# Optimization experiments

Measured on AMD Instinct MI355X. Metric: run time of the kernel, lower is better.

## Reference

```python
import jax, jax.numpy as jnp
import numpy as np

B, T, D = 512, 720, 774
P, H, E = 128, 128, 64


def setup_inputs() -> dict:
    key = jax.random.key(0)
    ks = jax.random.split(key, 24)
    x = jax.random.normal(ks[0], (B, T, D), jnp.float32)
    # emulate days with no news (all-zero rows) so has_news/recency are non-trivial
    news_mask = jax.random.bernoulli(ks[1], 0.35, (B, T, 1)).astype(jnp.float32)
    x = x * news_mask

    def w(k, shape, s=0.05):
        return jax.random.normal(k, shape, jnp.float32) * s

    return {
        "x": x,
        "w_proj": w(ks[2], (D + 2, P)), "b_proj": jnp.zeros((P,), jnp.float32),
        "ln_g": jnp.ones((P,), jnp.float32), "ln_b": jnp.zeros((P,), jnp.float32),
        # LSTM params stored as (in, 4H) / (H, 4H); torch gate order i,f,g,o
        "wih0": w(ks[3], (P, 4 * H)), "whh0": w(ks[4], (H, 4 * H)),
        "bih0": jnp.zeros((4 * H,), jnp.float32), "bhh0": jnp.zeros((4 * H,), jnp.float32).at[H:2 * H].set(1.0),
        "wih1": w(ks[5], (H, 4 * H)), "whh1": w(ks[6], (H, 4 * H)),
        "bih1": jnp.zeros((4 * H,), jnp.float32), "bhh1": jnp.zeros((4 * H,), jnp.float32).at[H:2 * H].set(1.0),
        "w_e1": w(ks[7], (H, H)), "b_e1": jnp.zeros((H,), jnp.float32),
        "w_e2": w(ks[8], (H, E)), "b_e2": jnp.zeros((E,), jnp.float32),
        "w_r": w(ks[9], (H, H // 2)), "b_r": jnp.zeros((H // 2,), jnp.float32),
        "w_o": w(ks[10], (H // 2, 1)), "b_o": jnp.zeros((1,), jnp.float32),
        "w_s": w(ks[11], (H, 1)),
    }


def _lstm_layer(inp, Wih, Whh, bih, bhh):
    # inp: (B, T, Din) -> (B, T, H). Precompute input projection once (GEMM),
    # scan only the recurrent part.
    b = inp.shape[0]
    h_dim = Whh.shape[0]
    pre = jnp.swapaxes(inp, 0, 1) @ Wih + bih + bhh  # (T, B, 4H)

    def step(carry, pt):
        h, c = carry
        g = pt + h @ Whh
        i, f, gg, o = jnp.split(g, 4, axis=-1)
        c = jax.nn.sigmoid(f) * c + jax.nn.sigmoid(i) * jnp.tanh(gg)
        h = jax.nn.sigmoid(o) * jnp.tanh(c)
        return (h, c), h

    init = (jnp.zeros((b, h_dim), inp.dtype), jnp.zeros((b, h_dim), inp.dtype))
    _, hs = jax.lax.scan(step, init, pre)
    return jnp.swapaxes(hs, 0, 1)  # (B, T, H)


def reference(x, w_proj, b_proj, ln_g, ln_b,
              wih0, whh0, bih0, bhh0, wih1, whh1, bih1, bhh1,
              w_e1, b_e1, w_e2, b_e2, w_r, b_r, w_o, b_o, w_s):
    t = x.shape[1]
    has = (jnp.sum(jnp.abs(x), axis=-1, keepdims=True) > 1e-6).astype(x.dtype)  # (B,T,1)
    # recency: days since last news / T -- the 720-step python loop is exactly
    # a reset-cumsum == (t - last_news_index)/T with last index from a cummax
    t_idx = jnp.arange(t, dtype=x.dtype)[None, :, None]
    last = jax.lax.cummax(jnp.where(has > 0.5, t_idx, jnp.float32(-1.0)), axis=1)
    rec = jnp.clip((t_idx - last) / t, 0.0, 1.0)

    xa = jnp.concatenate([x, has, rec], axis=-1)  # (B,T,D+2)
    h = jax.nn.gelu(xa @ w_proj + b_proj, approximate=False)  # dropout=eval no-op
    mu = jnp.mean(h, axis=-1, keepdims=True)
    var = jnp.var(h, axis=-1, keepdims=True)
    h = (h - mu) / jnp.sqrt(var + 1e-5) * ln_g + ln_b

    h = _lstm_layer(h, wih0, whh0, bih0, bhh0)
    h = _lstm_layer(h, wih1, whh1, bih1, bhh1)
    last_h = h[:, -1, :]  # (B,H)

    emb = jnp.tanh(jax.nn.gelu(last_h @ w_e1 + b_e1, approximate=False) @ w_e2 + b_e2)
    hr = jax.nn.gelu(last_h @ w_r + b_r, approximate=False)
    pred = (hr @ w_o + b_o + last_h @ w_s)[:, 0]
    return pred, emb
```

## Files before the change

### kernel.cpp

```cpp
#include <hip/hip_runtime.h>
#include <math.h>

#define BB 512
#define TT 720
#define DD 774
#define PP 128
#define HH 128
#define GG 512
#define DP2 776
#define TAB 721

__device__ __forceinline__ float gelu_f(float v){
    return 0.5f*v*(1.0f + erff(v*0.70710678118654752f));
}
__device__ __forceinline__ float sig_f(float v){
    return 1.0f/(1.0f + __expf(-v));
}

__global__ void k_zero(float* __restrict__ p, int n){
    int i = blockIdx.x*256 + threadIdx.x;
    if (i < n) p[i] = 0.f;
}

__global__ __launch_bounds__(256) void k_has(const float* __restrict__ x, float* __restrict__ has){
    int wid  = blockIdx.x*4 + (threadIdx.x >> 6);
    int lane = threadIdx.x & 63;
    const float2* row = reinterpret_cast<const float2*>(x + (size_t)wid*DD);
    float s = 0.f;
    #pragma unroll
    for (int i=0;i<6;i++){ float2 v = row[lane + i*64]; s += fabsf(v.x)+fabsf(v.y); }
    if (lane < 3){ float2 v = row[384 + lane]; s += fabsf(v.x)+fabsf(v.y); }
    #pragma unroll
    for (int off=32; off; off>>=1) s += __shfl_down(s, off, 64);
    if (lane == 0) has[wid] = (s > 1e-6f) ? 1.0f : 0.0f;
}

__global__ void k_rec(const float* __restrict__ has, int* __restrict__ recIdx,
                      int* __restrict__ cnt_bc, int Tc, int NC){
    int b = blockIdx.x*64 + threadIdx.x;
    if (b >= BB) return;
    const float* hp = has + (size_t)b*TT;
    int* rp = recIdx + (size_t)b*TT;
    int last = -1, cl = 0, c = 0;
    for (int t=0;t<TT;t++){
        if (t == (c+1)*Tc){ cnt_bc[b*NC + c] = cl; cl = 0; c++; }
        if (hp[t] > 0.5f){ last = t; cl++; }
        rp[t] = t - last;
    }
    cnt_bc[b*NC + c] = cl;
}

__global__ __launch_bounds__(512) void k_scan(const int* __restrict__ cnt_bc, int* __restrict__ base_bc,
                                              int* __restrict__ cntTotal, int NC){
    int c = blockIdx.x;
    int b = threadIdx.x;
    int v = cnt_bc[b*NC + c];
    int lane = b & 63, w = b >> 6;
    int xv = v;
    #pragma unroll
    for (int off=1; off<64; off<<=1){
        int y = __shfl_up(xv, off, 64);
        if (lane >= off) xv += y;
    }
    __shared__ int wsums[8];
    if (lane == 63) wsums[w] = xv;
    __syncthreads();
    if (b == 0){
        int run = 0;
        #pragma unroll
        for (int i=0;i<8;i++){ int tv = wsums[i]; wsums[i] = run; run += tv; }
        cntTotal[c] = run;
    }
    __syncthreads();
    base_bc[b*NC + c] = wsums[w] + xv - v;
}

__global__ void k_pos(const float* __restrict__ has, const int* __restrict__ base_bc,
                      int* __restrict__ posIdx, int* __restrict__ list, int Tc, int NC){
    int b = blockIdx.x*64 + threadIdx.x;
    if (b >= BB) return;
    const float* hp = has + (size_t)b*TT;
    int c = 0;
    int pos = base_bc[b*NC + 0];
    for (int t=0;t<TT;t++){
        if (t == (c+1)*Tc){ c++; pos = base_bc[b*NC + c]; }
        int r = b*TT + t;
        if (hp[t] > 0.5f){
            posIdx[r] = pos;
            list[(size_t)c*((size_t)BB*Tc) + pos] = r;
            pos++;
        } else {
            posIdx[r] = -1;
        }
    }
}

__global__ __launch_bounds__(128) void k_tab1(const float* __restrict__ wp, const float* __restrict__ bp,
        const float* __restrict__ lng, const float* __restrict__ lnb, float* __restrict__ tab1){
    int k = blockIdx.x, j = threadIdx.x;
    float rec = (float)k * (1.0f/720.0f);
    float v = gelu_f(rec * wp[775*PP + j] + bp[j]);
    int lane = j & 63, w = j >> 6;
    __shared__ float red[2];
    float s = v;
    #pragma unroll
    for (int off=32; off; off>>=1) s += __shfl_xor(s, off, 64);
    if (lane == 0) red[w] = s;
    __syncthreads();
    float mu = (red[0] + red[1]) * (1.0f/128.0f);
    __syncthreads();
    float d = v - mu, s2 = d*d;
    #pragma unroll
    for (int off=32; off; off>>=1) s2 += __shfl_xor(s2, off, 64);
    if (lane == 0) red[w] = s2;
    __syncthreads();
    float var = (red[0] + red[1]) * (1.0f/128.0f);
    tab1[k*PP + j] = d * rsqrtf(var + 1e-5f) * lng[j] + lnb[j];
}

__global__ __launch_bounds__(512) void k_tab2(const float* __restrict__ tab1, const float* __restrict__ wih,
        const float* __restrict__ bih, const float* __restrict__ bhh, float* __restrict__ tab2){
    int k = blockIdx.x, j = threadIdx.x;
    __shared__ float hrow[PP];
    if (j < PP) hrow[j] = tab1[k*PP + j];
    __syncthreads();
    float acc = bih[j] + bhh[j];
    #pragma unroll
    for (int kk=0; kk<PP; kk++) acc += hrow[kk]*wih[kk*GG + j];
    tab2[(size_t)k*GG + j] = acc;
}

__global__ __launch_bounds__(256) void k_proj(const float* __restrict__ x,
        const float* __restrict__ wp, const float* __restrict__ bp,
        const float* __restrict__ lng, const float* __restrict__ lnb,
        const int* __restrict__ listc, const int* __restrict__ cntPtr,
        float* __restrict__ h0c){
    int nc = cntPtr[0];
    int base = blockIdx.x*16;
    if (base >= nc) return;
    int nrows = min(16, nc - base);
    __shared__ float xs[16][DP2];
    __shared__ float hls[16][PP];
    __shared__ float mvs[16][2];
    const int tid = threadIdx.x;
    for (int rr=0; rr<16; rr++){
        if (rr < nrows){
            int row = listc[base + rr];
            const float* xr = x + (size_t)row*DD;
            for (int d = tid; d < DD; d += 256) xs[rr][d] = xr[d];
            if (tid == 0){ xs[rr][774] = 1.0f; xs[rr][775] = 0.0f; }
        }
    }
    __syncthreads();
    int col = tid & 127, rg = tid >> 7;
    float acc[8];
    #pragma unroll
    for (int r=0;r<8;r++) acc[r] = bp[col];
    const float* wcol = wp + col;
    for (int d=0; d<DP2; d+=4){
        float w0 = wcol[(d+0)*PP], w1 = wcol[(d+1)*PP], w2 = wcol[(d+2)*PP], w3 = wcol[(d+3)*PP];
        #pragma unroll
        for (int r=0;r<8;r++){
            float4 xv = *reinterpret_cast<const float4*>(&xs[rg*8 + r][d]);
            acc[r] = fmaf(xv.x, w0, acc[r]);
            acc[r] = fmaf(xv.y, w1, acc[r]);
            acc[r] = fmaf(xv.z, w2, acc[r]);
            acc[r] = fmaf(xv.w, w3, acc[r]);
        }
    }
    #pragma unroll
    for (int r=0;r<8;r++){ acc[r] = gelu_f(acc[r]); hls[rg*8 + r][col] = acc[r]; }
    __syncthreads();
    int w = tid >> 6, lane = tid & 63;
    for (int rr = w*4; rr < w*4 + 4; rr++){
        float s = hls[rr][lane] + hls[rr][lane + 64];
        #pragma unroll
        for (int off=32; off; off>>=1) s += __shfl_xor(s, off, 64);
        float mu = s * (1.0f/128.0f);
        float d0 = hls[rr][lane]-mu, d1 = hls[rr][lane+64]-mu;
        float s2 = d0*d0 + d1*d1;
        #pragma unroll
        for (int off=32; off; off>>=1) s2 += __shfl_xor(s2, off, 64);
        if (lane == 0){ mvs[rr][0] = mu; mvs[rr][1] = rsqrtf(s2*(1.0f/128.0f) + 1e-5f); }
    }
    __syncthreads();
    float g = lng[col], bb = lnb[col];
    #pragma unroll
    for (int r=0;r<8;r++){
        int rr = rg*8 + r;
        if (base + rr < nc){
            float o = (acc[r] - mvs[rr][0]) * mvs[rr][1] * g + bb;
            h0c[(size_t)(base+rr)*PP + col] = o;
        }
    }
}

__global__ __launch_bounds__(512) void k_pre(const float* __restrict__ inM,
        const float* __restrict__ wih, const float* __restrict__ bih, const float* __restrict__ bhh,
        const int* __restrict__ cntPtr, int fixedCount, float* __restrict__ outPre){
    int nc = cntPtr ? cntPtr[0] : fixedCount;
    int base = blockIdx.x*32;
    if (base >= nc) return;
    __shared__ float hs[32][PP];
    int tid = threadIdx.x;
    for (int i = tid; i < 32*PP; i += 512){
        int rr = i >> 7;
        if (base + rr < nc) hs[rr][i & 127] = inM[(size_t)(base+rr)*PP + (i & 127)];
    }
    __syncthreads();
    float bias = bih[tid] + bhh[tid];
    float acc[32];
    #pragma unroll
    for (int r=0;r<32;r++) acc[r] = bias;
    const float* wc = wih + tid;
    for (int k=0;k<PP;k+=4){
        float w0 = wc[(k+0)*GG], w1 = wc[(k+1)*GG], w2 = wc[(k+2)*GG], w3 = wc[(k+3)*GG];
        #pragma unroll
        for (int r=0;r<32;r++){
            float4 hv = *reinterpret_cast<const float4*>(&hs[r][k]);
            acc[r] = fmaf(hv.x, w0, acc[r]);
            acc[r] = fmaf(hv.y, w1, acc[r]);
            acc[r] = fmaf(hv.z, w2, acc[r]);
            acc[r] = fmaf(hv.w, w3, acc[r]);
        }
    }
    #pragma unroll
    for (int r=0;r<32;r++)
        if (base + r < nc) outPre[(size_t)(base+r)*GG + tid] = acc[r];
}

__global__ __launch_bounds__(512, 2) void k_lstm(
    const float* __restrict__ whh, const float* __restrict__ pre,
    const float* __restrict__ pretab, const int* __restrict__ posIdx,
    const int* __restrict__ recIdx, float* __restrict__ hState, float* __restrict__ cState,
    float* __restrict__ hsOut, int t0, int Tc, int layer)
{
    int b = blockIdx.x;
    int j = threadIdx.x;
    float w[128];
    #pragma unroll
    for (int k=0;k<128;k++) w[k] = whh[k*GG + j];
    __shared__ float hbuf[HH];
    __shared__ float hprev[HH];
    __shared__ float gbuf[GG];
    if (j < HH) hbuf[j] = hState[b*HH + j];
    float c_ = (j < HH) ? cState[b*HH + j] : 0.f;
    __syncthreads();
    for (int t = t0; t < t0 + Tc; t++){
        if (hsOut && t > t0 && j >= 128 && j < 256)
            hsOut[((size_t)(t-1-t0)*BB + b)*HH + (j-128)] = hprev[j-128];
        float p0;
        if (layer == 0){
            int pos = posIdx[(size_t)b*TT + t];
            const float* src = (pos >= 0) ? (pre + (size_t)pos*GG)
                                          : (pretab + (size_t)recIdx[(size_t)b*TT + t]*GG);
            p0 = src[j];
        } else {
            p0 = pre[((size_t)(t-t0)*BB + b)*GG + j];
        }
        float a0=0.f, a1=0.f, a2=0.f, a3=0.f;
        #pragma unroll
        for (int k=0;k<128;k+=16){
            float4 h0v = *reinterpret_cast<const float4*>(&hbuf[k]);
            float4 h1v = *reinterpret_cast<const float4*>(&hbuf[k+4]);
            float4 h2v = *reinterpret_cast<const float4*>(&hbuf[k+8]);
            float4 h3v = *reinterpret_cast<const float4*>(&hbuf[k+12]);
            a0 = fmaf(h0v.x, w[k+0],  a0); a0 = fmaf(h0v.y, w[k+1],  a0);
            a0 = fmaf(h0v.z, w[k+2],  a0); a0 = fmaf(h0v.w, w[k+3],  a0);
            a1 = fmaf(h1v.x, w[k+4],  a1); a1 = fmaf(h1v.y, w[k+5],  a1);
            a1 = fmaf(h1v.z, w[k+6],  a1); a1 = fmaf(h1v.w, w[k+7],  a1);
            a2 = fmaf(h2v.x, w[k+8],  a2); a2 = fmaf(h2v.y, w[k+9],  a2);
            a2 = fmaf(h2v.z, w[k+10], a2); a2 = fmaf(h2v.w, w[k+11], a2);
            a3 = fmaf(h3v.x, w[k+12], a3); a3 = fmaf(h3v.y, w[k+13], a3);
            a3 = fmaf(h3v.z, w[k+14], a3); a3 = fmaf(h3v.w, w[k+15], a3);
        }
        gbuf[j] = p0 + ((a0+a1)+(a2+a3));
        __syncthreads();
        if (j < HH){
            float gi = gbuf[j], gf = gbuf[HH+j], gg = gbuf[2*HH+j], go = gbuf[3*HH+j];
            c_ = sig_f(gf)*c_ + sig_f(gi)*tanhf(gg);
            float hn = sig_f(go)*tanhf(c_);
            hbuf[j] = hn;
            hprev[j] = hn;
        }
        __syncthreads();
    }
    if (hsOut && j >= 128 && j < 256)
        hsOut[((size_t)(Tc-1)*BB + b)*HH + (j-128)] = hprev[j-128];
    if (j < HH){ hState[b*HH + j] = hbuf[j]; cState[b*HH + j] = c_; }
}

__global__ __launch_bounds__(128) void k_head(const float* __restrict__ hS,
        const float* __restrict__ we1, const float* __restrict__ be1,
        const float* __restrict__ we2, const float* __restrict__ be2,
        const float* __restrict__ wr,  const float* __restrict__ br,
        const float* __restrict__ wo,  const float* __restrict__ bo,
        const float* __restrict__ wsv, float* __restrict__ out){
    int b = blockIdx.x, j = threadIdx.x;
    __shared__ float lh[128], e1[128], hr[64];
    lh[j] = hS[b*128 + j];
    __syncthreads();
    float acc = be1[j];
    #pragma unroll
    for (int k=0;k<128;k++) acc += lh[k]*we1[k*128 + j];
    e1[j] = gelu_f(acc);
    if (j < 64){
        float a2 = br[j];
        #pragma unroll
        for (int k=0;k<128;k++) a2 += lh[k]*wr[k*64 + j];
        hr[j] = gelu_f(a2);
    }
    __syncthreads();
    if (j < 64){
        float a3 = be2[j];
        #pragma unroll
        for (int k=0;k<128;k++) a3 += e1[k]*we2[k*64 + j];
        out[BB + b*64 + j] = tanhf(a3);
        float p = hr[j]*wo[j] + lh[j]*wsv[j] + lh[j+64]*wsv[j+64];
        #pragma unroll
        for (int off=32; off; off>>=1) p += __shfl_down(p, off, 64);
        if (j == 0) out[b] = p + bo[0];
    }
}

extern "C" void kernel_launch(void* const* d_in, const int* in_sizes, int n_in,
                              void* d_out, int out_size, void* d_ws, size_t ws_size,
                              hipStream_t stream) {
    const float* x     = (const float*)d_in[0];
    const float* wproj = (const float*)d_in[1];
    const float* bproj = (const float*)d_in[2];
    const float* lng   = (const float*)d_in[3];
    const float* lnb   = (const float*)d_in[4];
    const float* wih0  = (const float*)d_in[5];
    const float* whh0  = (const float*)d_in[6];
    const float* bih0  = (const float*)d_in[7];
    const float* bhh0  = (const float*)d_in[8];
    const float* wih1  = (const float*)d_in[9];
    const float* whh1  = (const float*)d_in[10];
    const float* bih1  = (const float*)d_in[11];
    const float* bhh1  = (const float*)d_in[12];
    const float* we1   = (const float*)d_in[13];
    const float* be1   = (const float*)d_in[14];
    const float* we2   = (const float*)d_in[15];
    const float* be2   = (const float*)d_in[16];
    const float* wr    = (const float*)d_in[17];
    const float* br    = (const float*)d_in[18];
    const float* wo    = (const float*)d_in[19];
    const float* bo    = (const float*)d_in[20];
    const float* wsv   = (const float*)d_in[21];
    float* out = (float*)d_out;

    const size_t BT = (size_t)BB*TT;
    static const int cands[12] = {90,60,45,30,20,15,10,6,5,3,2,1};
    size_t offs[12];
    auto plan = [&](int tc, size_t* o)->size_t{
        size_t NCc = (size_t)(TT / tc);
        size_t cur = 0;
        auto take = [&](size_t bytes){ size_t r = cur; cur = (cur + bytes + 255) & ~(size_t)255; return r; };
        o[0]  = take(BT*4);
        o[1]  = take(BT*4);
        o[2]  = take(BT*4);
        o[3]  = take(BT*4);
        o[4]  = take((size_t)BB*NCc*4);
        o[5]  = take((size_t)BB*NCc*4);
        o[6]  = take(NCc*4);
        o[7]  = take((size_t)TAB*PP*4);
        o[8]  = take((size_t)TAB*GG*4);
        o[9]  = take((size_t)4*BB*HH*4);
        o[10] = take((size_t)BB*tc*PP*4);
        o[11] = take((size_t)BB*tc*GG*4);
        return cur;
    };
    int Tc = 1;
    for (int ci=0; ci<12; ci++){
        if (plan(cands[ci], offs) <= ws_size){ Tc = cands[ci]; break; }
    }
    plan(Tc, offs);
    char* wsb = (char*)d_ws;
    float* f_has    = (float*)(wsb + offs[0]);
    int*   i_rec    = (int*)  (wsb + offs[1]);
    int*   i_pos    = (int*)  (wsb + offs[2]);
    int*   i_list   = (int*)  (wsb + offs[3]);
    int*   i_cntbc  = (int*)  (wsb + offs[4]);
    int*   i_basebc = (int*)  (wsb + offs[5]);
    int*   i_cnt    = (int*)  (wsb + offs[6]);
    float* f_tab1   = (float*)(wsb + offs[7]);
    float* f_tab2   = (float*)(wsb + offs[8]);
    float* f_st     = (float*)(wsb + offs[9]);
    float* f_h0     = (float*)(wsb + offs[10]);
    float* f_pre    = (float*)(wsb + offs[11]);
    const int NC = TT / Tc;

    float* st_h0 = f_st;
    float* st_c0 = f_st + (size_t)BB*HH;
    float* st_h1 = f_st + (size_t)2*BB*HH;
    float* st_c1 = f_st + (size_t)3*BB*HH;

    { int n = 4*BB*HH; k_zero<<<(n+255)/256, 256, 0, stream>>>(f_st, n); }
    k_has <<<(int)(BT/4), 256, 0, stream>>>(x, f_has);
    k_rec <<<(BB+63)/64, 64, 0, stream>>>(f_has, i_rec, i_cntbc, Tc, NC);
    k_scan<<<NC, 512, 0, stream>>>(i_cntbc, i_basebc, i_cnt, NC);
    k_pos <<<(BB+63)/64, 64, 0, stream>>>(f_has, i_basebc, i_pos, i_list, Tc, NC);
    k_tab1<<<TAB, 128, 0, stream>>>(wproj, bproj, lng, lnb, f_tab1);
    k_tab2<<<TAB, 512, 0, stream>>>(f_tab1, wih0, bih0, bhh0, f_tab2);

    const int rowsPerChunk = BB*Tc;
    for (int c=0; c<NC; c++){
        const int* listc = i_list + (size_t)c*rowsPerChunk;
        k_proj<<<(rowsPerChunk+15)/16, 256, 0, stream>>>(x, wproj, bproj, lng, lnb,
                listc, i_cnt + c, f_h0);
        k_pre <<<(rowsPerChunk+31)/32, 512, 0, stream>>>(f_h0, wih0, bih0, bhh0,
                i_cnt + c, 0, f_pre);
        k_lstm<<<BB, 512, 0, stream>>>(whh0, f_pre, f_tab2, i_pos, i_rec,
                st_h0, st_c0, f_h0, c*Tc, Tc, 0);
        k_pre <<<(rowsPerChunk+31)/32, 512, 0, stream>>>(f_h0, wih1, bih1, bhh1,
                nullptr, rowsPerChunk, f_pre);
        k_lstm<<<BB, 512, 0, stream>>>(whh1, f_pre, nullptr, nullptr, nullptr,
                st_h1, st_c1, nullptr, c*Tc, Tc, 1);
    }
    k_head<<<BB, 128, 0, stream>>>(st_h1, we1, be1, we2, be2, wr, br, wo, bo, wsv, out);
}
```

Measured before the change: 7.928 ms.

## Process two batch rows per LSTM block to reuse register-resident Whh

The recurrent LSTM kernel now handles two batch elements per 512-thread block, so each thread's 128 register-held Whh weights are applied to both hidden states per step. Grid size halves, the weight load per batch halves, and step-level synchronisation is shared across two sequences. The trade-offs are fewer blocks in flight (256 on a many-CU GPU) and a dropped min-blocks launch bound, which may change register allocation and occupancy. Gate activations now use 256 threads instead of 128.

```diff
diff --git a/kernel.cpp b/kernel.cpp
--- a/kernel.cpp
+++ b/kernel.cpp
@@ -229,65 +229,75 @@
         if (base + r < nc) outPre[(size_t)(base+r)*GG + tid] = acc[r];
 }
 
-__global__ __launch_bounds__(512, 2) void k_lstm(
+__global__ __launch_bounds__(512) void k_lstm2(
     const float* __restrict__ whh, const float* __restrict__ pre,
     const float* __restrict__ pretab, const int* __restrict__ posIdx,
     const int* __restrict__ recIdx, float* __restrict__ hState, float* __restrict__ cState,
     float* __restrict__ hsOut, int t0, int Tc, int layer)
 {
-    int b = blockIdx.x;
-    int j = threadIdx.x;
+    const int b0 = blockIdx.x*2, b1 = b0 + 1;
+    const int j = threadIdx.x;
     float w[128];
     #pragma unroll
     for (int k=0;k<128;k++) w[k] = whh[k*GG + j];
-    __shared__ float hbuf[HH];
-    __shared__ float hprev[HH];
-    __shared__ float gbuf[GG];
-    if (j < HH) hbuf[j] = hState[b*HH + j];
-    float c_ = (j < HH) ? cState[b*HH + j] : 0.f;
+    __shared__ float h0s[HH], h1s[HH];
+    __shared__ float g0s[GG], g1s[GG];
+    __shared__ float hp0[HH], hp1[HH];
+    float c_ = 0.f;
+    if (j < HH){ h0s[j] = hState[b0*HH + j]; c_ = cState[b0*HH + j]; }
+    else if (j < 2*HH){ h1s[j-HH] = hState[b1*HH + (j-HH)]; c_ = cState[b1*HH + (j-HH)]; }
     __syncthreads();
     for (int t = t0; t < t0 + Tc; t++){
-        if (hsOut && t > t0 && j >= 128 && j < 256)
-            hsOut[((size_t)(t-1-t0)*BB + b)*HH + (j-128)] = hprev[j-128];
-        float p0;
+        if (hsOut && t > t0){
+            if (j >= 256 && j < 384)      hsOut[((size_t)(t-1-t0)*BB + b0)*HH + (j-256)] = hp0[j-256];
+            else if (j >= 384)            hsOut[((size_t)(t-1-t0)*BB + b1)*HH + (j-384)] = hp1[j-384];
+        }
+        float p0, p1;
         if (layer == 0){
-            int pos = posIdx[(size_t)b*TT + t];
-            const float* src = (pos >= 0) ? (pre + (size_t)pos*GG)
-                                          : (pretab + (size_t)recIdx[(size_t)b*TT + t]*GG);
-            p0 = src[j];
+            int q0 = posIdx[(size_t)b0*TT + t];
+            int q1 = posIdx[(size_t)b1*TT + t];
+            const float* s0 = (q0 >= 0) ? (pre + (size_t)q0*GG)
+                                        : (pretab + (size_t)recIdx[(size_t)b0*TT + t]*GG);
+            const float* s1 = (q1 >= 0) ? (pre + (size_t)q1*GG)
+                                        : (pretab + (size_t)recIdx[(size_t)b1*TT + t]*GG);
+            p0 = s0[j]; p1 = s1[j];
         } else {
-            p0 = pre[((size_t)(t-t0)*BB + b)*GG + j];
-        }
-        float a0=0.f, a1=0.f, a2=0.f, a3=0.f;
-        #pragma unroll
-        for (int k=0;k<128;k+=16){
-            float4 h0v = *reinterpret_cast<const float4*>(&hbuf[k]);
-            float4 h1v = *reinterpret_cast<const float4*>(&hbuf[k+4]);
-            float4 h2v = *reinterpret_cast<const float4*>(&hbuf[k+8]);
-            float4 h3v = *reinterpret_cast<const float4*>(&hbuf[k+12]);
-            a0 = fmaf(h0v.x, w[k+0],  a0); a0 = fmaf(h0v.y, w[k+1],  a0);
-            a0 = fmaf(h0v.z, w[k+2],  a0); a0 = fmaf(h0v.w, w[k+3],  a0);
-            a1 = fmaf(h1v.x, w[k+4],  a1); a1 = fmaf(h1v.y, w[k+5],  a1);
-            a1 = fmaf(h1v.z, w[k+6],  a1); a1 = fmaf(h1v.w, w[k+7],  a1);
-            a2 = fmaf(h2v.x, w[k+8],  a2); a2 = fmaf(h2v.y, w[k+9],  a2);
-            a2 = fmaf(h2v.z, w[k+10], a2); a2 = fmaf(h2v.w, w[k+11], a2);
-            a3 = fmaf(h3v.x, w[k+12], a3); a3 = fmaf(h3v.y, w[k+13], a3);
-            a3 = fmaf(h3v.z, w[k+14], a3); a3 = fmaf(h3v.w, w[k+15], a3);
-        }
-        gbuf[j] = p0 + ((a0+a1)+(a2+a3));
+            p0 = pre[((size_t)(t-t0)*BB + b0)*GG + j];
+            p1 = pre[((size_t)(t-t0)*BB + b1)*GG + j];
+        }
+        float a00=0.f, a01=0.f, a10=0.f, a11=0.f;
+        #pragma unroll
+        for (int k=0;k<128;k+=4){
+            float4 x0 = *reinterpret_cast<const float4*>(&h0s[k]);
+            float4 y0 = *reinterpret_cast<const float4*>(&h1s[k]);
+            a00 = fmaf(x0.x, w[k+0], a00); a01 = fmaf(x0.y, w[k+1], a01);
+            a00 = fmaf(x0.z, w[k+2], a00); a01 = fmaf(x0.w, w[k+3], a01);
+            a10 = fmaf(y0.x, w[k+0], a10); a11 = fmaf(y0.y, w[k+1], a11);
+            a10 = fmaf(y0.z, w[k+2], a10); a11 = fmaf(y0.w, w[k+3], a11);
+        }
+        g0s[j] = p0 + (a00 + a01);
+        g1s[j] = p1 + (a10 + a11);
         __syncthreads();
         if (j < HH){
-            float gi = gbuf[j], gf = gbuf[HH+j], gg = gbuf[2*HH+j], go = gbuf[3*HH+j];
+            float gi = g0s[j], gf = g0s[HH+j], gg = g0s[2*HH+j], go = g0s[3*HH+j];
             c_ = sig_f(gf)*c_ + sig_f(gi)*tanhf(gg);
             float hn = sig_f(go)*tanhf(c_);
-            hbuf[j] = hn;
-            hprev[j] = hn;
+            h0s[j] = hn; hp0[j] = hn;
+        } else if (j < 2*HH){
+            int jj = j - HH;
+            float gi = g1s[jj], gf = g1s[HH+jj], gg = g1s[2*HH+jj], go = g1s[3*HH+jj];
+            c_ = sig_f(gf)*c_ + sig_f(gi)*tanhf(gg);
+            float hn = sig_f(go)*tanhf(c_);
+            h1s[jj] = hn; hp1[jj] = hn;
         }
         __syncthreads();
     }
-    if (hsOut && j >= 128 && j < 256)
-        hsOut[((size_t)(Tc-1)*BB + b)*HH + (j-128)] = hprev[j-128];
-    if (j < HH){ hState[b*HH + j] = hbuf[j]; cState[b*HH + j] = c_; }
+    if (hsOut){
+        if (j >= 256 && j < 384)      hsOut[((size_t)(Tc-1)*BB + b0)*HH + (j-256)] = hp0[j-256];
+        else if (j >= 384)            hsOut[((size_t)(Tc-1)*BB + b1)*HH + (j-384)] = hp1[j-384];
+    }
+    if (j < HH){ hState[b0*HH + j] = h0s[j]; cState[b0*HH + j] = c_; }
+    else if (j < 2*HH){ hState[b1*HH + (j-HH)] = h1s[j-HH]; cState[b1*HH + (j-HH)] = c_; }
 }
 
 __global__ __launch_bounds__(128) void k_head(const float* __restrict__ hS,
@@ -411,11 +421,11 @@
                 listc, i_cnt + c, f_h0);
         k_pre <<<(rowsPerChunk+31)/32, 512, 0, stream>>>(f_h0, wih0, bih0, bhh0,
                 i_cnt + c, 0, f_pre);
-        k_lstm<<<BB, 512, 0, stream>>>(whh0, f_pre, f_tab2, i_pos, i_rec,
+        k_lstm2<<<BB/2, 512, 0, stream>>>(whh0, f_pre, f_tab2, i_pos, i_rec,
                 st_h0, st_c0, f_h0, c*Tc, Tc, 0);
         k_pre <<<(rowsPerChunk+31)/32, 512, 0, stream>>>(f_h0, wih1, bih1, bhh1,
                 nullptr, rowsPerChunk, f_pre);
-        k_lstm<<<BB, 512, 0, stream>>>(whh1, f_pre, nullptr, nullptr, nullptr,
+        k_lstm2<<<BB/2, 512, 0, stream>>>(whh1, f_pre, nullptr, nullptr, nullptr,
                 st_h1, st_c1, nullptr, c*Tc, Tc, 1);
     }
     k_head<<<BB, 128, 0, stream>>>(st_h1, we1, be1, we2, be2, wr, br, wo, bo, wsv, out);
```

After: 7.888 ms. About the same (-0.5%).
